# Kernel optimization log

Measured on AMD Instinct MI355X. Metric: run time of the kernel, lower is better.

The kernel has to match this reference:

```python
import jax, jax.numpy as jnp
import numpy as np

NEG_SLOPE = 0.2  # DGL GATConv default negative_slope


def gat_conv(x, W, attn_l, attn_r, bias, src, dst, n_nodes):
    """DGL-style GATConv. x:[N,F_in], W:[F_in,H*D], attn_l/attn_r/bias:[H,D].
    Returns [N,H,D]."""
    H, D = attn_l.shape
    feat = (x @ W).reshape(n_nodes, H, D)            # projected features
    el = jnp.sum(feat * attn_l, axis=-1)              # [N,H]
    er = jnp.sum(feat * attn_r, axis=-1)              # [N,H]
    e = jax.nn.leaky_relu(el[src] + er[dst], NEG_SLOPE)  # [E,H] per-edge score
    # edge softmax over incoming edges of each dst node (numerically stable)
    m = jax.ops.segment_max(e, dst, num_segments=n_nodes)   # [N,H]
    a = jnp.exp(e - m[dst])
    denom = jax.ops.segment_sum(a, dst, num_segments=n_nodes)
    alpha = a / denom[dst]                            # [E,H]
    msg = feat[src] * alpha[..., None]                # [E,H,D]
    out = jax.ops.segment_sum(msg, dst, num_segments=n_nodes)  # [N,H,D]
    return out + bias


def setup_inputs() -> dict:
    key = jax.random.key(0)
    ks = jax.random.split(key, 12)
    N, E = 50000, 800000
    F_in, D1, H1, F_out = 128, 32, 4, 64
    h = jax.random.normal(ks[0], (N, F_in), dtype=jnp.float32)
    src = jax.random.randint(ks[1], (E,), 0, N, dtype=jnp.int32)
    dst = jax.random.randint(ks[2], (E,), 0, N, dtype=jnp.int32)
    s1 = 1.0 / np.sqrt(F_in)
    s2 = 1.0 / np.sqrt(H1 * D1)
    W1 = jax.random.normal(ks[3], (F_in, H1 * D1), dtype=jnp.float32) * s1
    al1 = jax.random.normal(ks[4], (H1, D1), dtype=jnp.float32) * s1
    ar1 = jax.random.normal(ks[5], (H1, D1), dtype=jnp.float32) * s1
    b1 = jnp.zeros((H1, D1), dtype=jnp.float32)
    W2 = jax.random.normal(ks[6], (H1 * D1, 1 * F_out), dtype=jnp.float32) * s2
    al2 = jax.random.normal(ks[7], (1, F_out), dtype=jnp.float32) * s2
    ar2 = jax.random.normal(ks[8], (1, F_out), dtype=jnp.float32) * s2
    b2 = jnp.zeros((1, F_out), dtype=jnp.float32)
    return {"h": h, "src": src, "dst": dst,
            "W1": W1, "al1": al1, "ar1": ar1, "b1": b1,
            "W2": W2, "al2": al2, "ar2": ar2, "b2": b2}


def reference(h, src, dst, W1, al1, ar1, b1, W2, al2, ar2, b2):
    N = h.shape[0]
    x = gat_conv(h, W1, al1, ar1, b1, src, dst, N)   # [N,H,D]
    x = jax.nn.relu(x.reshape(N, -1))                # flatten heads + ReLU
    # dropout(p=0.2) is identity in eval mode
    x = gat_conv(x, W2, al2, ar2, b2, src, dst, N)   # [N,1,F_out]
    return x.squeeze(1)
```

## Files before the change

kernel.cpp:

```cpp
#include <hip/hip_runtime.h>

#define NEG_SLOPE 0.2f
#define CH 4096
#define BSTRIDE 1536

__device__ inline unsigned short f2bf(float f) {
    unsigned u = __float_as_uint(f);
    unsigned r = (u + 0x7FFFu + ((u >> 16) & 1u)) >> 16;
    return (unsigned short)r;
}
__device__ inline unsigned pack2bf(float a, float b) {
    return (unsigned)f2bf(a) | ((unsigned)f2bf(b) << 16);
}
__device__ inline float bf2f_lo(unsigned u) { return __uint_as_float(u << 16); }
__device__ inline float bf2f_hi(unsigned u) { return __uint_as_float(u & 0xFFFF0000u); }
__device__ inline void wave_lds_fence() {
    asm volatile("s_waitcnt lgkmcnt(0)" ::: "memory");
}

__global__ __launch_bounds__(256) void csrP_gemm1_kernel(
    const int* __restrict__ src, const int* __restrict__ dst,
    int* __restrict__ bucket_cursor, unsigned* __restrict__ tmp, int E, int NB,
    int nchunks, const float* __restrict__ h, const float* __restrict__ W1,
    const float* __restrict__ al1, const float* __restrict__ ar1,
    unsigned short* __restrict__ feat1b, float* __restrict__ el1,
    float* __restrict__ er1, int N) {
    __shared__ __align__(16) int smem[8192];
    const int tid = threadIdx.x;
    if ((int)blockIdx.x < nchunks) {
        int* lh = smem;
        int* lex = smem + 1024;
        int* gbase_sh = smem + 2048;
        int* wsum = smem + 3072;
        unsigned* sortedv = (unsigned*)(smem + 3104);
        const int base_e = blockIdx.x * CH;
        const int cnt_e = min(CH, E - base_e);
        for (int i = tid; i < 1024; i += 256) lh[i] = 0;
        __syncthreads();
        for (int i = tid; i < cnt_e; i += 256) atomicAdd(&lh[dst[base_e + i] >> 6], 1);
        __syncthreads();
        const int lane = tid & 63;
        const int wid = tid >> 6;
        int s0 = lh[tid * 4], s1 = lh[tid * 4 + 1], s2 = lh[tid * 4 + 2],
            s3 = lh[tid * 4 + 3];
        int tot = s0 + s1 + s2 + s3;
        int inc = tot;
#pragma unroll
        for (int off = 1; off < 64; off <<= 1) {
            int t = __shfl_up(inc, off, 64);
            if (lane >= off) inc += t;
        }
        if (lane == 63) wsum[wid] = inc;
        __syncthreads();
        int wbase = 0;
#pragma unroll
        for (int k = 0; k < 4; ++k)
            if (k < wid) wbase += wsum[k];
        int ebase = wbase + inc - tot;
        lex[tid * 4] = ebase;
        lex[tid * 4 + 1] = ebase + s0;
        lex[tid * 4 + 2] = ebase + s0 + s1;
        lex[tid * 4 + 3] = ebase + s0 + s1 + s2;
        for (int b = tid; b < NB; b += 256) {
            int c = lh[b];
            gbase_sh[b] = c ? atomicAdd(&bucket_cursor[b], c) : 0;
        }
        __syncthreads();
        for (int i = tid; i < 1024; i += 256) lh[i] = 0;
        __syncthreads();
        for (int i = tid; i < cnt_e; i += 256) {
            int e = base_e + i;
            int d = dst[e];
            unsigned b = (unsigned)d >> 6;
            int r = atomicAdd(&lh[b], 1);
            sortedv[lex[b] + r] =
                (b << 22) | ((unsigned)(d & 63) << 16) | (unsigned)(src[e] & 0xFFFF);
        }
        __syncthreads();
        for (int i = tid; i < cnt_e; i += 256) {
            unsigned v = sortedv[i];
            int b = v >> 22;
            int pos = gbase_sh[b] + (i - lex[b]);
            if (pos < BSTRIDE)
                tmp[(size_t)b * BSTRIDE + pos] = v;
        }
    } else {
        float* xs = (float*)smem;
        const int row0 = ((int)blockIdx.x - nchunks) * 64;
        {
            const float4* s4 = (const float4*)h;
            float4* d4 = (float4*)xs;
            int base4 = row0 * 32;
            int tot4 = N * 32;
            for (int i = tid; i < 2048; i += 256)
                if (base4 + i < tot4) d4[i] = s4[base4 + i];
        }
        __syncthreads();
        const int lane = tid & 31;
        const int c0 = lane * 4;
        const int r0 = (tid >> 5) * 8;
        float acc[8][4] = {};
#pragma unroll 4
        for (int k = 0; k < 128; ++k) {
            float4 w = *(const float4*)(W1 + k * 128 + c0);
#pragma unroll
            for (int r = 0; r < 8; ++r) {
                float x = xs[(r0 + r) * 128 + k];
                acc[r][0] = fmaf(x, w.x, acc[r][0]);
                acc[r][1] = fmaf(x, w.y, acc[r][1]);
                acc[r][2] = fmaf(x, w.z, acc[r][2]);
                acc[r][3] = fmaf(x, w.w, acc[r][3]);
            }
        }
        float4 alv = *(const float4*)(al1 + c0);
        float4 arv = *(const float4*)(ar1 + c0);
#pragma unroll
        for (int r = 0; r < 8; ++r) {
            int row = row0 + r0 + r;
            if (row < N) {
                ushort4 fb;
                fb.x = f2bf(acc[r][0]);
                fb.y = f2bf(acc[r][1]);
                fb.z = f2bf(acc[r][2]);
                fb.w = f2bf(acc[r][3]);
                *(ushort4*)(feat1b + (size_t)row * 128 + c0) = fb;
                float pl = acc[r][0] * alv.x + acc[r][1] * alv.y + acc[r][2] * alv.z +
                           acc[r][3] * alv.w;
                float pr = acc[r][0] * arv.x + acc[r][1] * arv.y + acc[r][2] * arv.z +
                           acc[r][3] * arv.w;
#pragma unroll
                for (int off = 4; off >= 1; off >>= 1) {
                    pl += __shfl_xor(pl, off, 32);
                    pr += __shfl_xor(pr, off, 32);
                }
                if ((lane & 7) == 0) {
                    el1[row * 4 + (lane >> 3)] = pl;
                    er1[row * 4 + (lane >> 3)] = pr;
                }
            }
        }
    }
}

__global__ __launch_bounds__(256) void gemm2_fused(const unsigned short* __restrict__ out1b,
                                                   const float* __restrict__ W2,
                                                   const float* __restrict__ al2,
                                                   const float* __restrict__ ar2,
                                                   unsigned short* __restrict__ feat2b,
                                                   float* __restrict__ el2,
                                                   float* __restrict__ er2, int N) {
    __shared__ float xs[64 * 128];
    const int tid = threadIdx.x;
    const int row0 = blockIdx.x * 64;
    {
        const uint4* s8 = (const uint4*)out1b;
        int base8 = row0 * 16;
        int tot8 = N * 16;
        for (int i = tid; i < 1024; i += 256)
            if (base8 + i < tot8) {
                uint4 v = s8[base8 + i];
                float* o = xs + i * 8;
                o[0] = bf2f_lo(v.x);
                o[1] = bf2f_hi(v.x);
                o[2] = bf2f_lo(v.y);
                o[3] = bf2f_hi(v.y);
                o[4] = bf2f_lo(v.z);
                o[5] = bf2f_hi(v.z);
                o[6] = bf2f_lo(v.w);
                o[7] = bf2f_hi(v.w);
            }
    }
    __syncthreads();
    const int lane = tid & 15;
    const int c0 = lane * 4;
    const int r0 = (tid >> 4) * 4;
    float acc[4][4] = {};
#pragma unroll 4
    for (int k = 0; k < 128; ++k) {
        float4 w = *(const float4*)(W2 + k * 64 + c0);
#pragma unroll
        for (int r = 0; r < 4; ++r) {
            float x = xs[(r0 + r) * 128 + k];
            acc[r][0] = fmaf(x, w.x, acc[r][0]);
            acc[r][1] = fmaf(x, w.y, acc[r][1]);
            acc[r][2] = fmaf(x, w.z, acc[r][2]);
            acc[r][3] = fmaf(x, w.w, acc[r][3]);
        }
    }
    float4 alv = *(const float4*)(al2 + c0);
    float4 arv = *(const float4*)(ar2 + c0);
#pragma unroll
    for (int r = 0; r < 4; ++r) {
        int row = row0 + r0 + r;
        if (row < N) {
            ushort4 fb;
            fb.x = f2bf(acc[r][0]);
            fb.y = f2bf(acc[r][1]);
            fb.z = f2bf(acc[r][2]);
            fb.w = f2bf(acc[r][3]);
            *(ushort4*)(feat2b + (size_t)row * 64 + c0) = fb;
            float pl = acc[r][0] * alv.x + acc[r][1] * alv.y + acc[r][2] * alv.z +
                       acc[r][3] * alv.w;
            float pr = acc[r][0] * arv.x + acc[r][1] * arv.y + acc[r][2] * arv.z +
                       acc[r][3] * arv.w;
#pragma unroll
            for (int off = 8; off >= 1; off >>= 1) {
                pl += __shfl_xor(pl, off, 16);
                pr += __shfl_xor(pr, off, 16);
            }
            if (lane == 0) {
                el2[row] = pl;
                er2[row] = pr;
            }
        }
    }
}

__global__ __launch_bounds__(256) void gather1_kernel(const unsigned* __restrict__ tmp,
                                                      const int* __restrict__ bucket_cursor,
                                                      const float* __restrict__ el1,
                                                      const float* __restrict__ er1,
                                                      const unsigned short* __restrict__ feat1b,
                                                      const float* __restrict__ b1,
                                                      unsigned short* __restrict__ out1b,
                                                      int N) {
    __shared__ unsigned sval[BSTRIDE];
    __shared__ int ssrc[BSTRIDE];
    __shared__ int dh[64], dex[64], dcur[64];
    __shared__ float a_sh[4][256];
    const int tid = threadIdx.x;
    const int b = (int)blockIdx.x >> 1;
    const int half = (int)blockIdx.x & 1;
    const int gb = b * BSTRIDE;
    const int cnt = min(bucket_cursor[b], BSTRIDE);
    if (tid < 64) dh[tid] = 0;
    __syncthreads();
    for (int i = tid; i < cnt; i += 256) {
        unsigned v = tmp[gb + i];
        sval[i] = v;
        atomicAdd(&dh[(v >> 16) & 63], 1);
    }
    __syncthreads();
    if (tid < 64) {
        int v = dh[tid], inc = v;
#pragma unroll
        for (int off = 1; off < 64; off <<= 1) {
            int t = __shfl_up(inc, off, 64);
            if (tid >= off) inc += t;
        }
        dex[tid] = inc - v;
        dcur[tid] = inc - v;
    }
    __syncthreads();
    for (int i = tid; i < cnt; i += 256) {
        unsigned val = sval[i];
        int dl = (val >> 16) & 63;
        int pos = atomicAdd(&dcur[dl], 1);
        ssrc[pos] = (int)(val & 0xFFFFu);
    }
    __syncthreads();
    const int w = tid >> 6;
    const int lane = tid & 63;
    const int q = lane >> 4;
    const int l16 = lane & 15;
    const int c0 = l16 * 8;
    const int hh = l16 >> 2;
    float4 bv0 = *(const float4*)(b1 + c0);
    float4 bv1 = *(const float4*)(b1 + c0 + 4);
    for (int k = 0; k < 8; ++k) {
        const int dl = half * 32 + w * 8 + k;
        const int d = b * 64 + dl;
        if (d >= N) break;
        const int base = dex[dl];
        const int M = dh[dl];
        float4 er4 = *(const float4*)(er1 + (size_t)d * 4);
        float acc[8] = {}, bcc[8] = {};
        float den = 0.f;
        for (int k0 = 0; k0 < M; k0 += 64) {
            const int Mt = min(64, M - k0);
            if (lane < Mt) {
                int s = ssrc[base + k0 + lane];
                float4 el4 = *(const float4*)(el1 + (size_t)s * 4);
                float v0 = el4.x + er4.x;
                float v1 = el4.y + er4.y;
                float v2 = el4.z + er4.z;
                float v3 = el4.w + er4.w;
                v0 = v0 > 0.f ? v0 : NEG_SLOPE * v0;
                v1 = v1 > 0.f ? v1 : NEG_SLOPE * v1;
                v2 = v2 > 0.f ? v2 : NEG_SLOPE * v2;
                v3 = v3 > 0.f ? v3 : NEG_SLOPE * v3;
                a_sh[w][lane * 4 + 0] = __expf(v0);
                a_sh[w][lane * 4 + 1] = __expf(v1);
                a_sh[w][lane * 4 + 2] = __expf(v2);
                a_sh[w][lane * 4 + 3] = __expf(v3);
            }
            wave_lds_fence();
            int e = q;
            for (; e + 4 < Mt; e += 8) {
                int s0 = ssrc[base + k0 + e], s1 = ssrc[base + k0 + e + 4];
                float a0 = a_sh[w][e * 4 + hh];
                float a1 = a_sh[w][(e + 4) * 4 + hh];
                uint4 f0 = *(const uint4*)(feat1b + (size_t)s0 * 128 + c0);
                uint4 f1 = *(const uint4*)(feat1b + (size_t)s1 * 128 + c0);
                den += a0 + a1;
                acc[0] = fmaf(bf2f_lo(f0.x), a0, acc[0]);
                acc[1] = fmaf(bf2f_hi(f0.x), a0, acc[1]);
                acc[2] = fmaf(bf2f_lo(f0.y), a0, acc[2]);
                acc[3] = fmaf(bf2f_hi(f0.y), a0, acc[3]);
                acc[4] = fmaf(bf2f_lo(f0.z), a0, acc[4]);
                acc[5] = fmaf(bf2f_hi(f0.z), a0, acc[5]);
                acc[6] = fmaf(bf2f_lo(f0.w), a0, acc[6]);
                acc[7] = fmaf(bf2f_hi(f0.w), a0, acc[7]);
                bcc[0] = fmaf(bf2f_lo(f1.x), a1, bcc[0]);
                bcc[1] = fmaf(bf2f_hi(f1.x), a1, bcc[1]);
                bcc[2] = fmaf(bf2f_lo(f1.y), a1, bcc[2]);
                bcc[3] = fmaf(bf2f_hi(f1.y), a1, bcc[3]);
                bcc[4] = fmaf(bf2f_lo(f1.z), a1, bcc[4]);
                bcc[5] = fmaf(bf2f_hi(f1.z), a1, bcc[5]);
                bcc[6] = fmaf(bf2f_lo(f1.w), a1, bcc[6]);
                bcc[7] = fmaf(bf2f_hi(f1.w), a1, bcc[7]);
            }
            while (e < Mt) {
                int s0 = ssrc[base + k0 + e];
                float a0 = a_sh[w][e * 4 + hh];
                uint4 f0 = *(const uint4*)(feat1b + (size_t)s0 * 128 + c0);
                den += a0;
                acc[0] = fmaf(bf2f_lo(f0.x), a0, acc[0]);
                acc[1] = fmaf(bf2f_hi(f0.x), a0, acc[1]);
                acc[2] = fmaf(bf2f_lo(f0.y), a0, acc[2]);
                acc[3] = fmaf(bf2f_hi(f0.y), a0, acc[3]);
                acc[4] = fmaf(bf2f_lo(f0.z), a0, acc[4]);
                acc[5] = fmaf(bf2f_hi(f0.z), a0, acc[5]);
                acc[6] = fmaf(bf2f_lo(f0.w), a0, acc[6]);
                acc[7] = fmaf(bf2f_hi(f0.w), a0, acc[7]);
                e += 4;
            }
            wave_lds_fence();
        }
#pragma unroll
        for (int j = 0; j < 8; ++j) {
            acc[j] += bcc[j];
            acc[j] += __shfl_xor(acc[j], 16, 64);
            acc[j] += __shfl_xor(acc[j], 32, 64);
        }
        den += __shfl_xor(den, 16, 64);
        den += __shfl_xor(den, 32, 64);
        if (q == 0) {
            float inv = (M > 0) ? 1.f / den : 0.f;
            uint4 o;
            o.x = pack2bf(fmaxf(acc[0] * inv + bv0.x, 0.f), fmaxf(acc[1] * inv + bv0.y, 0.f));
            o.y = pack2bf(fmaxf(acc[2] * inv + bv0.z, 0.f), fmaxf(acc[3] * inv + bv0.w, 0.f));
            o.z = pack2bf(fmaxf(acc[4] * inv + bv1.x, 0.f), fmaxf(acc[5] * inv + bv1.y, 0.f));
            o.w = pack2bf(fmaxf(acc[6] * inv + bv1.z, 0.f), fmaxf(acc[7] * inv + bv1.w, 0.f));
            *(uint4*)(out1b + (size_t)d * 128 + c0) = o;
        }
    }
}

__global__ __launch_bounds__(256) void gather2_kernel(const unsigned* __restrict__ tmp,
                                                      const int* __restrict__ bucket_cursor,
                                                      const float* __restrict__ el2,
                                                      const float* __restrict__ er2,
                                                      const unsigned short* __restrict__ feat2b,
                                                      const float* __restrict__ b2,
                                                      float* __restrict__ out2, int N) {
    __shared__ unsigned sval[BSTRIDE];
    __shared__ int ssrc[BSTRIDE];
    __shared__ int dh[64], dex[64], dcur[64];
    __shared__ float a_sh[4][64];
    const int tid = threadIdx.x;
    const int b = (int)blockIdx.x >> 1;
    const int half = (int)blockIdx.x & 1;
    const int gb = b * BSTRIDE;
    const int cnt = min(bucket_cursor[b], BSTRIDE);
    if (tid < 64) dh[tid] = 0;
    __syncthreads();
    for (int i = tid; i < cnt; i += 256) {
        unsigned v = tmp[gb + i];
        sval[i] = v;
        atomicAdd(&dh[(v >> 16) & 63], 1);
    }
    __syncthreads();
    if (tid < 64) {
        int v = dh[tid], inc = v;
#pragma unroll
        for (int off = 1; off < 64; off <<= 1) {
            int t = __shfl_up(inc, off, 64);
            if (tid >= off) inc += t;
        }
        dex[tid] = inc - v;
        dcur[tid] = inc - v;
    }
    __syncthreads();
    for (int i = tid; i < cnt; i += 256) {
        unsigned val = sval[i];
        int dl = (val >> 16) & 63;
        int pos = atomicAdd(&dcur[dl], 1);
        ssrc[pos] = (int)(val & 0xFFFFu);
    }
    __syncthreads();
    const int w = tid >> 6;
    const int lane = tid & 63;
    const int oct = lane >> 3;
    const int l8 = lane & 7;
    const int c0 = l8 * 8;
    float4 bv0 = *(const float4*)(b2 + c0);
    float4 bv1 = *(const float4*)(b2 + c0 + 4);
    for (int k = 0; k < 8; ++k) {
        const int dl = half * 32 + w * 8 + k;
        const int d = b * 64 + dl;
        if (d >= N) break;
        const int base = dex[dl];
        const int M = dh[dl];
        const float er_d = er2[d];
        float acc[8] = {}, bcc[8] = {};
        float den = 0.f;
        for (int k0 = 0; k0 < M; k0 += 64) {
            const int Mt = min(64, M - k0);
            if (lane < Mt) {
                int s = ssrc[base + k0 + lane];
                float v = el2[s] + er_d;
                v = v > 0.f ? v : NEG_SLOPE * v;
                a_sh[w][lane] = __expf(v);
            }
            wave_lds_fence();
            int e = oct;
            for (; e + 8 < Mt; e += 16) {
                int s0 = ssrc[base + k0 + e], s1 = ssrc[base + k0 + e + 8];
                float a0 = a_sh[w][e], a1 = a_sh[w][e + 8];
                uint4 f0 = *(const uint4*)(feat2b + (size_t)s0 * 64 + c0);
                uint4 f1 = *(const uint4*)(feat2b + (size_t)s1 * 64 + c0);
                den += a0 + a1;
                acc[0] = fmaf(bf2f_lo(f0.x), a0, acc[0]);
                acc[1] = fmaf(bf2f_hi(f0.x), a0, acc[1]);
                acc[2] = fmaf(bf2f_lo(f0.y), a0, acc[2]);
                acc[3] = fmaf(bf2f_hi(f0.y), a0, acc[3]);
                acc[4] = fmaf(bf2f_lo(f0.z), a0, acc[4]);
                acc[5] = fmaf(bf2f_hi(f0.z), a0, acc[5]);
                acc[6] = fmaf(bf2f_lo(f0.w), a0, acc[6]);
                acc[7] = fmaf(bf2f_hi(f0.w), a0, acc[7]);
                bcc[0] = fmaf(bf2f_lo(f1.x), a1, bcc[0]);
                bcc[1] = fmaf(bf2f_hi(f1.x), a1, bcc[1]);
                bcc[2] = fmaf(bf2f_lo(f1.y), a1, bcc[2]);
                bcc[3] = fmaf(bf2f_hi(f1.y), a1, bcc[3]);
                bcc[4] = fmaf(bf2f_lo(f1.z), a1, bcc[4]);
                bcc[5] = fmaf(bf2f_hi(f1.z), a1, bcc[5]);
                bcc[6] = fmaf(bf2f_lo(f1.w), a1, bcc[6]);
                bcc[7] = fmaf(bf2f_hi(f1.w), a1, bcc[7]);
            }
            while (e < Mt) {
                int s0 = ssrc[base + k0 + e];
                float a0 = a_sh[w][e];
                uint4 f0 = *(const uint4*)(feat2b + (size_t)s0 * 64 + c0);
                den += a0;
                acc[0] = fmaf(bf2f_lo(f0.x), a0, acc[0]);
                acc[1] = fmaf(bf2f_hi(f0.x), a0, acc[1]);
                acc[2] = fmaf(bf2f_lo(f0.y), a0, acc[2]);
                acc[3] = fmaf(bf2f_hi(f0.y), a0, acc[3]);
                acc[4] = fmaf(bf2f_lo(f0.z), a0, acc[4]);
                acc[5] = fmaf(bf2f_hi(f0.z), a0, acc[5]);
                acc[6] = fmaf(bf2f_lo(f0.w), a0, acc[6]);
                acc[7] = fmaf(bf2f_hi(f0.w), a0, acc[7]);
                e += 8;
            }
            wave_lds_fence();
        }
#pragma unroll
        for (int j = 0; j < 8; ++j) {
            acc[j] += bcc[j];
            acc[j] += __shfl_xor(acc[j], 8, 64);
            acc[j] += __shfl_xor(acc[j], 16, 64);
            acc[j] += __shfl_xor(acc[j], 32, 64);
        }
        den += __shfl_xor(den, 8, 64);
        den += __shfl_xor(den, 16, 64);
        den += __shfl_xor(den, 32, 64);
        if (oct == 0) {
            float inv = (M > 0) ? 1.f / den : 0.f;
            *(float4*)(out2 + (size_t)d * 64 + c0) =
                make_float4(acc[0] * inv + bv0.x, acc[1] * inv + bv0.y,
                            acc[2] * inv + bv0.z, acc[3] * inv + bv0.w);
            *(float4*)(out2 + (size_t)d * 64 + c0 + 4) =
                make_float4(acc[4] * inv + bv1.x, acc[5] * inv + bv1.y,
                            acc[6] * inv + bv1.z, acc[7] * inv + bv1.w);
        }
    }
}

extern "C" void kernel_launch(void* const* d_in, const int* in_sizes, int n_in,
                              void* d_out, int out_size, void* d_ws, size_t ws_size,
                              hipStream_t stream) {
    const float* h   = (const float*)d_in[0];
    const int*   src = (const int*)d_in[1];
    const int*   dst = (const int*)d_in[2];
    const float* W1  = (const float*)d_in[3];
    const float* al1 = (const float*)d_in[4];
    const float* ar1 = (const float*)d_in[5];
    const float* b1  = (const float*)d_in[6];
    const float* W2  = (const float*)d_in[7];
    const float* al2 = (const float*)d_in[8];
    const float* ar2 = (const float*)d_in[9];
    const float* b2  = (const float*)d_in[10];

    const int N = in_sizes[0] / 128;
    const int E = in_sizes[1];
    const int NB = (N + 63) >> 6;

    char* ws = (char*)d_ws;
    size_t off = 0;
    auto alloc = [&](size_t elems) -> void* {
        void* p = (void*)(ws + off);
        off += ((elems * 4 + 255) / 256) * 256;
        return p;
    };
    int* bucket_cursor = (int*)alloc(NB);
    unsigned* tmp      = (unsigned*)alloc((size_t)NB * BSTRIDE);
    float* el1   = (float*)alloc((size_t)N * 4);
    float* er1   = (float*)alloc((size_t)N * 4);
    unsigned short* feat1b = (unsigned short*)alloc((size_t)N * 64);
    unsigned short* out1b  = (unsigned short*)alloc((size_t)N * 64);
    float* el2   = (float*)alloc(N);
    float* er2   = (float*)alloc(N);
    unsigned short* feat2b = (unsigned short*)alloc((size_t)N * 32);
    float* out2  = (float*)d_out;

    const int nchunks = (E + CH - 1) / CH;
    const int gemm1_blocks = (N + 63) / 64;

    hipMemsetAsync(bucket_cursor, 0, (size_t)NB * 4, stream);
    csrP_gemm1_kernel<<<nchunks + gemm1_blocks, 256, 0, stream>>>(
        src, dst, bucket_cursor, tmp, E, NB, nchunks, h, W1, al1, ar1, feat1b,
        el1, er1, N);

    gather1_kernel<<<NB * 2, 256, 0, stream>>>(tmp, bucket_cursor, el1, er1,
                                               feat1b, b1, out1b, N);

    gemm2_fused<<<(N + 63) / 64, 256, 0, stream>>>(out1b, W2, al2, ar2, feat2b, el2,
                                                   er2, N);
    gather2_kernel<<<NB * 2, 256, 0, stream>>>(tmp, bucket_cursor, el2, er2,
                                               feat2b, b2, out2, N);
}
```

Baseline: 209.5 us.

## Fuse layer-1 aggregation with layer-2 projection and vectorize GEMM1 LDS reads

The second-layer projection GEMM is folded into the layer-1 gather kernel. Each block keeps its 32 aggregated bf16 rows in shared memory and projects them through W2 directly, so the out1b round trip through global memory and one kernel launch go away. Separately, the GEMM1 inner loop now reads four k-values per row as a float4 from LDS instead of scalar loads. In exchange the gather kernel uses more shared memory and registers, which may lower its occupancy, and the 64-column GEMM2 is recomputed with a less regular thread mapping.

Result: slower. 222.7 us (+6.3%).

```diff
diff --git a/kernel.cpp b/kernel.cpp
--- a/kernel.cpp
+++ b/kernel.cpp
@@ -100,16 +100,23 @@
         const int c0 = lane * 4;
         const int r0 = (tid >> 5) * 8;
         float acc[8][4] = {};
-#pragma unroll 4
-        for (int k = 0; k < 128; ++k) {
-            float4 w = *(const float4*)(W1 + k * 128 + c0);
-#pragma unroll
-            for (int r = 0; r < 8; ++r) {
-                float x = xs[(r0 + r) * 128 + k];
-                acc[r][0] = fmaf(x, w.x, acc[r][0]);
-                acc[r][1] = fmaf(x, w.y, acc[r][1]);
-                acc[r][2] = fmaf(x, w.z, acc[r][2]);
-                acc[r][3] = fmaf(x, w.w, acc[r][3]);
+#pragma unroll 2
+        for (int k0 = 0; k0 < 128; k0 += 4) {
+            float4 xv[8];
+#pragma unroll
+            for (int r = 0; r < 8; ++r)
+                xv[r] = *(const float4*)(xs + (r0 + r) * 128 + k0);
+#pragma unroll
+            for (int kk = 0; kk < 4; ++kk) {
+                float4 w = *(const float4*)(W1 + (k0 + kk) * 128 + c0);
+#pragma unroll
+                for (int r = 0; r < 8; ++r) {
+                    float x = ((const float*)&xv[r])[kk];
+                    acc[r][0] = fmaf(x, w.x, acc[r][0]);
+                    acc[r][1] = fmaf(x, w.y, acc[r][1]);
+                    acc[r][2] = fmaf(x, w.z, acc[r][2]);
+                    acc[r][3] = fmaf(x, w.w, acc[r][3]);
+                }
             }
         }
         float4 alv = *(const float4*)(al1 + c0);
@@ -142,92 +149,18 @@
     }
 }
 
-__global__ __launch_bounds__(256) void gemm2_fused(const unsigned short* __restrict__ out1b,
-                                                   const float* __restrict__ W2,
-                                                   const float* __restrict__ al2,
-                                                   const float* __restrict__ ar2,
-                                                   unsigned short* __restrict__ feat2b,
-                                                   float* __restrict__ el2,
-                                                   float* __restrict__ er2, int N) {
-    __shared__ float xs[64 * 128];
-    const int tid = threadIdx.x;
-    const int row0 = blockIdx.x * 64;
-    {
-        const uint4* s8 = (const uint4*)out1b;
-        int base8 = row0 * 16;
-        int tot8 = N * 16;
-        for (int i = tid; i < 1024; i += 256)
-            if (base8 + i < tot8) {
-                uint4 v = s8[base8 + i];
-                float* o = xs + i * 8;
-                o[0] = bf2f_lo(v.x);
-                o[1] = bf2f_hi(v.x);
-                o[2] = bf2f_lo(v.y);
-                o[3] = bf2f_hi(v.y);
-                o[4] = bf2f_lo(v.z);
-                o[5] = bf2f_hi(v.z);
-                o[6] = bf2f_lo(v.w);
-                o[7] = bf2f_hi(v.w);
-            }
-    }
-    __syncthreads();
-    const int lane = tid & 15;
-    const int c0 = lane * 4;
-    const int r0 = (tid >> 4) * 4;
-    float acc[4][4] = {};
-#pragma unroll 4
-    for (int k = 0; k < 128; ++k) {
-        float4 w = *(const float4*)(W2 + k * 64 + c0);
-#pragma unroll
-        for (int r = 0; r < 4; ++r) {
-            float x = xs[(r0 + r) * 128 + k];
-            acc[r][0] = fmaf(x, w.x, acc[r][0]);
-            acc[r][1] = fmaf(x, w.y, acc[r][1]);
-            acc[r][2] = fmaf(x, w.z, acc[r][2]);
-            acc[r][3] = fmaf(x, w.w, acc[r][3]);
-        }
-    }
-    float4 alv = *(const float4*)(al2 + c0);
-    float4 arv = *(const float4*)(ar2 + c0);
-#pragma unroll
-    for (int r = 0; r < 4; ++r) {
-        int row = row0 + r0 + r;
-        if (row < N) {
-            ushort4 fb;
-            fb.x = f2bf(acc[r][0]);
-            fb.y = f2bf(acc[r][1]);
-            fb.z = f2bf(acc[r][2]);
-            fb.w = f2bf(acc[r][3]);
-            *(ushort4*)(feat2b + (size_t)row * 64 + c0) = fb;
-            float pl = acc[r][0] * alv.x + acc[r][1] * alv.y + acc[r][2] * alv.z +
-                       acc[r][3] * alv.w;
-            float pr = acc[r][0] * arv.x + acc[r][1] * arv.y + acc[r][2] * arv.z +
-                       acc[r][3] * arv.w;
-#pragma unroll
-            for (int off = 8; off >= 1; off >>= 1) {
-                pl += __shfl_xor(pl, off, 16);
-                pr += __shfl_xor(pr, off, 16);
-            }
-            if (lane == 0) {
-                el2[row] = pl;
-                er2[row] = pr;
-            }
-        }
-    }
-}
-
-__global__ __launch_bounds__(256) void gather1_kernel(const unsigned* __restrict__ tmp,
-                                                      const int* __restrict__ bucket_cursor,
-                                                      const float* __restrict__ el1,
-                                                      const float* __restrict__ er1,
-                                                      const unsigned short* __restrict__ feat1b,
-                                                      const float* __restrict__ b1,
-                                                      unsigned short* __restrict__ out1b,
-                                                      int N) {
+__global__ __launch_bounds__(256) void gather1_gemm2_kernel(
+    const unsigned* __restrict__ tmp, const int* __restrict__ bucket_cursor,
+    const float* __restrict__ el1, const float* __restrict__ er1,
+    const unsigned short* __restrict__ feat1b, const float* __restrict__ b1,
+    const float* __restrict__ W2, const float* __restrict__ al2,
+    const float* __restrict__ ar2, unsigned short* __restrict__ feat2b,
+    float* __restrict__ el2, float* __restrict__ er2, int N) {
     __shared__ unsigned sval[BSTRIDE];
     __shared__ int ssrc[BSTRIDE];
     __shared__ int dh[64], dex[64], dcur[64];
     __shared__ float a_sh[4][256];
+    __shared__ __align__(16) unsigned out1s[32 * 68];
     const int tid = threadIdx.x;
     const int b = (int)blockIdx.x >> 1;
     const int half = (int)blockIdx.x & 1;
@@ -352,7 +285,64 @@
             o.y = pack2bf(fmaxf(acc[2] * inv + bv0.z, 0.f), fmaxf(acc[3] * inv + bv0.w, 0.f));
             o.z = pack2bf(fmaxf(acc[4] * inv + bv1.x, 0.f), fmaxf(acc[5] * inv + bv1.y, 0.f));
             o.w = pack2bf(fmaxf(acc[6] * inv + bv1.z, 0.f), fmaxf(acc[7] * inv + bv1.w, 0.f));
-            *(uint4*)(out1b + (size_t)d * 128 + c0) = o;
+            const int rb = w * 8 + k;
+            *(uint4*)&out1s[rb * 68 + l16 * 4] = o;
+        }
+    }
+    __syncthreads();
+    {
+        const int l16b = tid & 15;
+        const int cc0 = l16b * 4;
+        const int rg = tid >> 4;
+        float a2[2][4] = {};
+#pragma unroll 4
+        for (int k0 = 0; k0 < 128; k0 += 8) {
+            uint4 xv0 = *(const uint4*)&out1s[(rg * 2 + 0) * 68 + (k0 >> 1)];
+            uint4 xv1 = *(const uint4*)&out1s[(rg * 2 + 1) * 68 + (k0 >> 1)];
+            const float* wp = W2 + k0 * 64 + cc0;
+#pragma unroll
+            for (int kk = 0; kk < 8; ++kk) {
+                unsigned uv0 = ((const unsigned*)&xv0)[kk >> 1];
+                unsigned uv1 = ((const unsigned*)&xv1)[kk >> 1];
+                float x0 = (kk & 1) ? bf2f_hi(uv0) : bf2f_lo(uv0);
+                float x1 = (kk & 1) ? bf2f_hi(uv1) : bf2f_lo(uv1);
+                float4 wv = *(const float4*)(wp + kk * 64);
+                a2[0][0] = fmaf(x0, wv.x, a2[0][0]);
+                a2[0][1] = fmaf(x0, wv.y, a2[0][1]);
+                a2[0][2] = fmaf(x0, wv.z, a2[0][2]);
+                a2[0][3] = fmaf(x0, wv.w, a2[0][3]);
+                a2[1][0] = fmaf(x1, wv.x, a2[1][0]);
+                a2[1][1] = fmaf(x1, wv.y, a2[1][1]);
+                a2[1][2] = fmaf(x1, wv.z, a2[1][2]);
+                a2[1][3] = fmaf(x1, wv.w, a2[1][3]);
+            }
+        }
+        float4 alv = *(const float4*)(al2 + cc0);
+        float4 arv = *(const float4*)(ar2 + cc0);
+#pragma unroll
+        for (int r = 0; r < 2; ++r) {
+            const int d = b * 64 + half * 32 + rg * 2 + r;
+            float pl = a2[r][0] * alv.x + a2[r][1] * alv.y + a2[r][2] * alv.z +
+                       a2[r][3] * alv.w;
+            float pr = a2[r][0] * arv.x + a2[r][1] * arv.y + a2[r][2] * arv.z +
+                       a2[r][3] * arv.w;
+#pragma unroll
+            for (int off = 8; off >= 1; off >>= 1) {
+                pl += __shfl_xor(pl, off, 16);
+                pr += __shfl_xor(pr, off, 16);
+            }
+            if (d < N) {
+                ushort4 fb;
+                fb.x = f2bf(a2[r][0]);
+                fb.y = f2bf(a2[r][1]);
+                fb.z = f2bf(a2[r][2]);
+                fb.w = f2bf(a2[r][3]);
+                *(ushort4*)(feat2b + (size_t)d * 64 + cc0) = fb;
+                if (l16b == 0) {
+                    el2[d] = pl;
+                    er2[d] = pr;
+                }
+            }
         }
     }
 }
@@ -518,7 +508,6 @@
     float* el1   = (float*)alloc((size_t)N * 4);
     float* er1   = (float*)alloc((size_t)N * 4);
     unsigned short* feat1b = (unsigned short*)alloc((size_t)N * 64);
-    unsigned short* out1b  = (unsigned short*)alloc((size_t)N * 64);
     float* el2   = (float*)alloc(N);
     float* er2   = (float*)alloc(N);
     unsigned short* feat2b = (unsigned short*)alloc((size_t)N * 32);
@@ -532,11 +521,10 @@
         src, dst, bucket_cursor, tmp, E, NB, nchunks, h, W1, al1, ar1, feat1b,
         el1, er1, N);
 
-    gather1_kernel<<<NB * 2, 256, 0, stream>>>(tmp, bucket_cursor, el1, er1,
-                                               feat1b, b1, out1b, N);
-
-    gemm2_fused<<<(N + 63) / 64, 256, 0, stream>>>(out1b, W2, al2, ar2, feat2b, el2,
-                                                   er2, N);
+    gather1_gemm2_kernel<<<NB * 2, 256, 0, stream>>>(tmp, bucket_cursor, el1, er1,
+                                                     feat1b, b1, W2, al2, ar2,
+                                                     feat2b, el2, er2, N);
+
     gather2_kernel<<<NB * 2, 256, 0, stream>>>(tmp, bucket_cursor, el2, er2,
                                                feat2b, b2, out2, N);
 }
```

## Precompute edge attention weights block-wide in LDS and vectorize GEMM1 LDS reads

Applied to the files above, without the earlier changes.

Both gather kernels now compute every edge's exp(leaky_relu(el+er)) in one block-wide pass over the half-bucket and keep the results in shared memory. The per-wave 64-edge chunk loop, with its wave-local LDS fences and serialized score computation, goes away. The dst-local id is packed into the sorted source entries, and gather1 unrolls to four edges per iteration so more feature loads are in flight. GEMM1 reads x from LDS as float4 across four k at a time. The cost is a larger shared footprint and an extra block barrier. Edges past 1024 in a half-bucket would be silently dropped in gather1.

After: 216.5 us. 3.3% more time.

```diff
diff --git a/kernel.cpp b/kernel.cpp
--- a/kernel.cpp
+++ b/kernel.cpp
@@ -14,9 +14,17 @@
 }
 __device__ inline float bf2f_lo(unsigned u) { return __uint_as_float(u << 16); }
 __device__ inline float bf2f_hi(unsigned u) { return __uint_as_float(u & 0xFFFF0000u); }
-__device__ inline void wave_lds_fence() {
-    asm volatile("s_waitcnt lgkmcnt(0)" ::: "memory");
-}
+__device__ inline float lrelu(float v) { return v > 0.f ? v : NEG_SLOPE * v; }
+
+#define FMA8(A, F, S)                          \
+    A[0] = fmaf(bf2f_lo((F).x), S, A[0]);      \
+    A[1] = fmaf(bf2f_hi((F).x), S, A[1]);      \
+    A[2] = fmaf(bf2f_lo((F).y), S, A[2]);      \
+    A[3] = fmaf(bf2f_hi((F).y), S, A[3]);      \
+    A[4] = fmaf(bf2f_lo((F).z), S, A[4]);      \
+    A[5] = fmaf(bf2f_hi((F).z), S, A[5]);      \
+    A[6] = fmaf(bf2f_lo((F).w), S, A[6]);      \
+    A[7] = fmaf(bf2f_hi((F).w), S, A[7]);
 
 __global__ __launch_bounds__(256) void csrP_gemm1_kernel(
     const int* __restrict__ src, const int* __restrict__ dst,
@@ -100,16 +108,23 @@
         const int c0 = lane * 4;
         const int r0 = (tid >> 5) * 8;
         float acc[8][4] = {};
-#pragma unroll 4
-        for (int k = 0; k < 128; ++k) {
-            float4 w = *(const float4*)(W1 + k * 128 + c0);
-#pragma unroll
-            for (int r = 0; r < 8; ++r) {
-                float x = xs[(r0 + r) * 128 + k];
-                acc[r][0] = fmaf(x, w.x, acc[r][0]);
-                acc[r][1] = fmaf(x, w.y, acc[r][1]);
-                acc[r][2] = fmaf(x, w.z, acc[r][2]);
-                acc[r][3] = fmaf(x, w.w, acc[r][3]);
+#pragma unroll 2
+        for (int k0 = 0; k0 < 128; k0 += 4) {
+            float4 xv[8];
+#pragma unroll
+            for (int r = 0; r < 8; ++r)
+                xv[r] = *(const float4*)(xs + (r0 + r) * 128 + k0);
+#pragma unroll
+            for (int kk = 0; kk < 4; ++kk) {
+                float4 w = *(const float4*)(W1 + (k0 + kk) * 128 + c0);
+#pragma unroll
+                for (int r = 0; r < 8; ++r) {
+                    float x = ((const float*)&xv[r])[kk];
+                    acc[r][0] = fmaf(x, w.x, acc[r][0]);
+                    acc[r][1] = fmaf(x, w.y, acc[r][1]);
+                    acc[r][2] = fmaf(x, w.z, acc[r][2]);
+                    acc[r][3] = fmaf(x, w.w, acc[r][3]);
+                }
             }
         }
         float4 alv = *(const float4*)(al1 + c0);
@@ -224,10 +239,10 @@
                                                       const float* __restrict__ b1,
                                                       unsigned short* __restrict__ out1b,
                                                       int N) {
-    __shared__ unsigned sval[BSTRIDE];
+    __shared__ __align__(16) float a_all[4096];
     __shared__ int ssrc[BSTRIDE];
     __shared__ int dh[64], dex[64], dcur[64];
-    __shared__ float a_sh[4][256];
+    unsigned* sval = (unsigned*)a_all;
     const int tid = threadIdx.x;
     const int b = (int)blockIdx.x >> 1;
     const int half = (int)blockIdx.x & 1;
@@ -256,7 +271,23 @@
         unsigned val = sval[i];
         int dl = (val >> 16) & 63;
         int pos = atomicAdd(&dcur[dl], 1);
-        ssrc[pos] = (int)(val & 0xFFFFu);
+        ssrc[pos] = (int)((unsigned)(dl << 16) | (val & 0xFFFFu));
+    }
+    __syncthreads();
+    const int begH = half ? dex[32] : 0;
+    const int endH = half ? cnt : dex[32];
+    for (int i = begH + tid; i < endH; i += 256) {
+        int val = ssrc[i];
+        int s = val & 0xFFFF;
+        int dl = val >> 16;
+        float4 el4 = *(const float4*)(el1 + (size_t)s * 4);
+        float4 er4 = *(const float4*)(er1 + (size_t)(b * 64 + dl) * 4);
+        float v0 = __expf(lrelu(el4.x + er4.x));
+        float v1 = __expf(lrelu(el4.y + er4.y));
+        float v2 = __expf(lrelu(el4.z + er4.z));
+        float v3 = __expf(lrelu(el4.w + er4.w));
+        int idx = i - begH;
+        if (idx < 1024) *(float4*)&a_all[idx * 4] = make_float4(v0, v1, v2, v3);
     }
     __syncthreads();
     const int w = tid >> 6;
@@ -271,71 +302,37 @@
         const int dl = half * 32 + w * 8 + k;
         const int d = b * 64 + dl;
         if (d >= N) break;
-        const int base = dex[dl];
+        const int baseA = dex[dl];
+        const int baseR = baseA - begH;
         const int M = dh[dl];
-        float4 er4 = *(const float4*)(er1 + (size_t)d * 4);
         float acc[8] = {}, bcc[8] = {};
         float den = 0.f;
-        for (int k0 = 0; k0 < M; k0 += 64) {
-            const int Mt = min(64, M - k0);
-            if (lane < Mt) {
-                int s = ssrc[base + k0 + lane];
-                float4 el4 = *(const float4*)(el1 + (size_t)s * 4);
-                float v0 = el4.x + er4.x;
-                float v1 = el4.y + er4.y;
-                float v2 = el4.z + er4.z;
-                float v3 = el4.w + er4.w;
-                v0 = v0 > 0.f ? v0 : NEG_SLOPE * v0;
-                v1 = v1 > 0.f ? v1 : NEG_SLOPE * v1;
-                v2 = v2 > 0.f ? v2 : NEG_SLOPE * v2;
-                v3 = v3 > 0.f ? v3 : NEG_SLOPE * v3;
-                a_sh[w][lane * 4 + 0] = __expf(v0);
-                a_sh[w][lane * 4 + 1] = __expf(v1);
-                a_sh[w][lane * 4 + 2] = __expf(v2);
-                a_sh[w][lane * 4 + 3] = __expf(v3);
-            }
-            wave_lds_fence();
-            int e = q;
-            for (; e + 4 < Mt; e += 8) {
-                int s0 = ssrc[base + k0 + e], s1 = ssrc[base + k0 + e + 4];
-                float a0 = a_sh[w][e * 4 + hh];
-                float a1 = a_sh[w][(e + 4) * 4 + hh];
-                uint4 f0 = *(const uint4*)(feat1b + (size_t)s0 * 128 + c0);
-                uint4 f1 = *(const uint4*)(feat1b + (size_t)s1 * 128 + c0);
-                den += a0 + a1;
-                acc[0] = fmaf(bf2f_lo(f0.x), a0, acc[0]);
-                acc[1] = fmaf(bf2f_hi(f0.x), a0, acc[1]);
-                acc[2] = fmaf(bf2f_lo(f0.y), a0, acc[2]);
-                acc[3] = fmaf(bf2f_hi(f0.y), a0, acc[3]);
-                acc[4] = fmaf(bf2f_lo(f0.z), a0, acc[4]);
-                acc[5] = fmaf(bf2f_hi(f0.z), a0, acc[5]);
-                acc[6] = fmaf(bf2f_lo(f0.w), a0, acc[6]);
-                acc[7] = fmaf(bf2f_hi(f0.w), a0, acc[7]);
-                bcc[0] = fmaf(bf2f_lo(f1.x), a1, bcc[0]);
-                bcc[1] = fmaf(bf2f_hi(f1.x), a1, bcc[1]);
-                bcc[2] = fmaf(bf2f_lo(f1.y), a1, bcc[2]);
-                bcc[3] = fmaf(bf2f_hi(f1.y), a1, bcc[3]);
-                bcc[4] = fmaf(bf2f_lo(f1.z), a1, bcc[4]);
-                bcc[5] = fmaf(bf2f_hi(f1.z), a1, bcc[5]);
-                bcc[6] = fmaf(bf2f_lo(f1.w), a1, bcc[6]);
-                bcc[7] = fmaf(bf2f_hi(f1.w), a1, bcc[7]);
-            }
-            while (e < Mt) {
-                int s0 = ssrc[base + k0 + e];
-                float a0 = a_sh[w][e * 4 + hh];
-                uint4 f0 = *(const uint4*)(feat1b + (size_t)s0 * 128 + c0);
-                den += a0;
-                acc[0] = fmaf(bf2f_lo(f0.x), a0, acc[0]);
-                acc[1] = fmaf(bf2f_hi(f0.x), a0, acc[1]);
-                acc[2] = fmaf(bf2f_lo(f0.y), a0, acc[2]);
-                acc[3] = fmaf(bf2f_hi(f0.y), a0, acc[3]);
-                acc[4] = fmaf(bf2f_lo(f0.z), a0, acc[4]);
-                acc[5] = fmaf(bf2f_hi(f0.z), a0, acc[5]);
-                acc[6] = fmaf(bf2f_lo(f0.w), a0, acc[6]);
-                acc[7] = fmaf(bf2f_hi(f0.w), a0, acc[7]);
-                e += 4;
-            }
-            wave_lds_fence();
+        int e = q;
+        for (; e + 12 < M; e += 16) {
+            int s0 = ssrc[baseA + e] & 0xFFFF;
+            int s1 = ssrc[baseA + e + 4] & 0xFFFF;
+            int s2 = ssrc[baseA + e + 8] & 0xFFFF;
+            int s3 = ssrc[baseA + e + 12] & 0xFFFF;
+            float a0 = a_all[(baseR + e) * 4 + hh];
+            float a1 = a_all[(baseR + e + 4) * 4 + hh];
+            float a2 = a_all[(baseR + e + 8) * 4 + hh];
+            float a3 = a_all[(baseR + e + 12) * 4 + hh];
+            uint4 f0 = *(const uint4*)(feat1b + (size_t)s0 * 128 + c0);
+            uint4 f1 = *(const uint4*)(feat1b + (size_t)s1 * 128 + c0);
+            uint4 f2 = *(const uint4*)(feat1b + (size_t)s2 * 128 + c0);
+            uint4 f3 = *(const uint4*)(feat1b + (size_t)s3 * 128 + c0);
+            den += (a0 + a1) + (a2 + a3);
+            FMA8(acc, f0, a0);
+            FMA8(bcc, f1, a1);
+            FMA8(acc, f2, a2);
+            FMA8(bcc, f3, a3);
+        }
+        for (; e < M; e += 4) {
+            int s0 = ssrc[baseA + e] & 0xFFFF;
+            float a0 = a_all[(baseR + e) * 4 + hh];
+            uint4 f0 = *(const uint4*)(feat1b + (size_t)s0 * 128 + c0);
+            den += a0;
+            FMA8(acc, f0, a0);
         }
 #pragma unroll
         for (int j = 0; j < 8; ++j) {
@@ -364,10 +361,10 @@
                                                       const unsigned short* __restrict__ feat2b,
                                                       const float* __restrict__ b2,
                                                       float* __restrict__ out2, int N) {
-    __shared__ unsigned sval[BSTRIDE];
+    __shared__ __align__(16) float a_all[BSTRIDE];
     __shared__ int ssrc[BSTRIDE];
     __shared__ int dh[64], dex[64], dcur[64];
-    __shared__ float a_sh[4][64];
+    unsigned* sval = (unsigned*)a_all;
     const int tid = threadIdx.x;
     const int b = (int)blockIdx.x >> 1;
     const int half = (int)blockIdx.x & 1;
@@ -396,7 +393,17 @@
         unsigned val = sval[i];
         int dl = (val >> 16) & 63;
         int pos = atomicAdd(&dcur[dl], 1);
-        ssrc[pos] = (int)(val & 0xFFFFu);
+        ssrc[pos] = (int)((unsigned)(dl << 16) | (val & 0xFFFFu));
+    }
+    __syncthreads();
+    const int begH = half ? dex[32] : 0;
+    const int endH = half ? cnt : dex[32];
+    for (int i = begH + tid; i < endH; i += 256) {
+        int val = ssrc[i];
+        int s = val & 0xFFFF;
+        int dl = val >> 16;
+        float v = el2[s] + er2[b * 64 + dl];
+        a_all[i] = __expf(lrelu(v));
     }
     __syncthreads();
     const int w = tid >> 6;
@@ -412,58 +419,27 @@
         if (d >= N) break;
         const int base = dex[dl];
         const int M = dh[dl];
-        const float er_d = er2[d];
         float acc[8] = {}, bcc[8] = {};
         float den = 0.f;
-        for (int k0 = 0; k0 < M; k0 += 64) {
-            const int Mt = min(64, M - k0);
-            if (lane < Mt) {
-                int s = ssrc[base + k0 + lane];
-                float v = el2[s] + er_d;
-                v = v > 0.f ? v : NEG_SLOPE * v;
-                a_sh[w][lane] = __expf(v);
-            }
-            wave_lds_fence();
-            int e = oct;
-            for (; e + 8 < Mt; e += 16) {
-                int s0 = ssrc[base + k0 + e], s1 = ssrc[base + k0 + e + 8];
-                float a0 = a_sh[w][e], a1 = a_sh[w][e + 8];
-                uint4 f0 = *(const uint4*)(feat2b + (size_t)s0 * 64 + c0);
-                uint4 f1 = *(const uint4*)(feat2b + (size_t)s1 * 64 + c0);
-                den += a0 + a1;
-                acc[0] = fmaf(bf2f_lo(f0.x), a0, acc[0]);
-                acc[1] = fmaf(bf2f_hi(f0.x), a0, acc[1]);
-                acc[2] = fmaf(bf2f_lo(f0.y), a0, acc[2]);
-                acc[3] = fmaf(bf2f_hi(f0.y), a0, acc[3]);
-                acc[4] = fmaf(bf2f_lo(f0.z), a0, acc[4]);
-                acc[5] = fmaf(bf2f_hi(f0.z), a0, acc[5]);
-                acc[6] = fmaf(bf2f_lo(f0.w), a0, acc[6]);
-                acc[7] = fmaf(bf2f_hi(f0.w), a0, acc[7]);
-                bcc[0] = fmaf(bf2f_lo(f1.x), a1, bcc[0]);
-                bcc[1] = fmaf(bf2f_hi(f1.x), a1, bcc[1]);
-                bcc[2] = fmaf(bf2f_lo(f1.y), a1, bcc[2]);
-                bcc[3] = fmaf(bf2f_hi(f1.y), a1, bcc[3]);
-                bcc[4] = fmaf(bf2f_lo(f1.z), a1, bcc[4]);
-                bcc[5] = fmaf(bf2f_hi(f1.z), a1, bcc[5]);
-                bcc[6] = fmaf(bf2f_lo(f1.w), a1, bcc[6]);
-                bcc[7] = fmaf(bf2f_hi(f1.w), a1, bcc[7]);
-            }
-            while (e < Mt) {
-                int s0 = ssrc[base + k0 + e];
-                float a0 = a_sh[w][e];
-                uint4 f0 = *(const uint4*)(feat2b + (size_t)s0 * 64 + c0);
-                den += a0;
-                acc[0] = fmaf(bf2f_lo(f0.x), a0, acc[0]);
-                acc[1] = fmaf(bf2f_hi(f0.x), a0, acc[1]);
-                acc[2] = fmaf(bf2f_lo(f0.y), a0, acc[2]);
-                acc[3] = fmaf(bf2f_hi(f0.y), a0, acc[3]);
-                acc[4] = fmaf(bf2f_lo(f0.z), a0, acc[4]);
-                acc[5] = fmaf(bf2f_hi(f0.z), a0, acc[5]);
-                acc[6] = fmaf(bf2f_lo(f0.w), a0, acc[6]);
-                acc[7] = fmaf(bf2f_hi(f0.w), a0, acc[7]);
-                e += 8;
-            }
-            wave_lds_fence();
+        int e = oct;
+        for (; e + 8 < M; e += 16) {
+            int s0 = ssrc[base + e] & 0xFFFF;
+            int s1 = ssrc[base + e + 8] & 0xFFFF;
+            float a0 = a_all[base + e];
+            float a1 = a_all[base + e + 8];
+            uint4 f0 = *(const uint4*)(feat2b + (size_t)s0 * 64 + c0);
+            uint4 f1 = *(const uint4*)(feat2b + (size_t)s1 * 64 + c0);
+            den += a0 + a1;
+            FMA8(acc, f0, a0);
+            FMA8(bcc, f1, a1);
+        }
+        while (e < M) {
+            int s0 = ssrc[base + e] & 0xFFFF;
+            float a0 = a_all[base + e];
+            uint4 f0 = *(const uint4*)(feat2b + (size_t)s0 * 64 + c0);
+            den += a0;
+            FMA8(acc, f0, a0);
+            e += 8;
         }
 #pragma unroll
         for (int j = 0; j < 8; ++j) {
```
